# Kernel optimization log

Hardware: AMD Instinct MI355X
Metric: run time of the kernel (lower is better)

## Reference

```python
import math
import jax, jax.numpy as jnp
import numpy as np

B, S, D, H = 8, 512, 1024, 16
DH = D // H
NEG_BIG = -1.0e30  # stands in for torch's -np.inf (exp underflows to 0 identically)


def setup_inputs() -> dict:
    key0 = jax.random.key(0)
    ks = jax.random.split(key0, 20)
    n = lambda k, shp, s=1.0: jax.random.normal(k, shp, dtype=jnp.float32) * s
    inp = {}
    inp["query"] = n(ks[0], (B, S, D))
    inp["key"] = n(ks[1], (B, S, D))
    inp["value"] = n(ks[2], (B, S, D))
    # rel has exact zeros (they get masked to -10000 before its softmax)
    inp["rel"] = jax.random.randint(ks[3], (B, S, S), 0, 3).astype(jnp.float32)
    inp["timestamp"] = n(ks[4], (B, S, S))
    inp["l1"] = jnp.float32(0.3)
    inp["l2"] = jnp.float32(0.3)
    # causal mask: True = masked (future positions)
    inp["mask"] = jnp.broadcast_to(jnp.triu(jnp.ones((S, S), dtype=bool), k=1), (B, S, S))
    inp["encode_pos"] = 0
    # three qkv projection linears (total_size -> total_size)
    w = 1.0 / math.sqrt(D)
    inp["Wq"], inp["bq"] = n(ks[5], (D, D), w), jnp.zeros((D,), jnp.float32)
    inp["Wk"], inp["bk"] = n(ks[6], (D, D), w), jnp.zeros((D,), jnp.float32)
    inp["Wv"], inp["bv"] = n(ks[7], (D, D), w), jnp.zeros((D,), jnp.float32)
    # clip_factor / guessing_factor: Linear(head_size -> 1) applied to per-head key
    wh = 1.0 / math.sqrt(DH)
    inp["Wc"], inp["bc"] = n(ks[8], (1, DH), wh), jnp.zeros((1,), jnp.float32)
    inp["Wg"], inp["bg"] = n(ks[9], (1, DH), wh), jnp.zeros((1,), jnp.float32)
    return inp


def reference(query, key, value, rel, timestamp, l1, l2, mask, encode_pos,
              Wq, bq, Wk, bk, Wv, bv, Wc, bc, Wg, bg):
    b, s, d = query.shape
    dh = Wc.shape[1]
    h = d // dh

    def proj(x, W, bias):  # [b,s,d] -> [b,h,s,dh]
        return (x @ W.T + bias).reshape(b, s, h, dh).transpose(0, 2, 1, 3)

    q = proj(query, Wq, bq)
    k = proj(key, Wk, bk)
    v = proj(value, Wv, bv)

    m4 = mask[:, None]          # [b,1,s,s] broadcast over heads
    rel4 = rel[:, None]         # [b,1,s,s]
    ts4 = timestamp[:, None]    # [b,1,s,s]

    # relative softmax: zeros masked to -10000
    rel_attn = jax.nn.softmax(jnp.where(rel4 == 0, -10000.0, rel4), axis=-1)

    # scaled dot-product scores
    scores = jnp.einsum('bhqd,bhkd->bhqk', q, k) / math.sqrt(dh)
    scores = jnp.where(m4, -1.0e9, scores)

    # clip / guessing factors from per-head key -> [b,h,s,1]
    cf = k @ Wc.T + bc
    gf = k @ Wg.T + bg
    R1 = jax.nn.sigmoid(gf - cf) + gf

    # time-decay softmax
    time_stamp = jnp.where(m4, NEG_BIG, jnp.exp(-jnp.abs(ts4)))
    Rs = time_stamp + R1  # [b,h,s,s] (R1 broadcasts over last axis, as in torch)

    prob_attn = jax.nn.softmax(scores, axis=-1)
    time_attn = jax.nn.softmax(Rs, axis=-1)
    prob_attn = (1.0 - l2) * prob_attn + l2 * time_attn
    prob_attn = (1.0 - l1) * prob_attn + l1 * rel_attn

    out = jnp.einsum('bhqk,bhkd->bhqd', prob_attn, v)
    out = out.transpose(0, 2, 1, 3).reshape(b, s, d)
    return out, prob_attn
```

## Files before the change

kernel.cpp:

```cpp
#include <hip/hip_runtime.h>
#include <math.h>

typedef __attribute__((ext_vector_type(8))) short short8;
typedef __attribute__((ext_vector_type(4))) float f32x4;

#define B_  8
#define S_  512
#define D_  1024
#define H_  16
#define DH_ 64

__device__ __forceinline__ unsigned short f2bf(float f) {
    unsigned int u = __float_as_uint(f);
    u += 0x7FFFu + ((u >> 16) & 1u);
    return (unsigned short)(u >> 16);
}
__device__ __forceinline__ float bf2f(unsigned short u) {
    return __uint_as_float(((unsigned int)u) << 16);
}
__device__ __forceinline__ void gload_lds16(const void* g, void* l) {
    __builtin_amdgcn_global_load_lds(
        (const __attribute__((address_space(1))) unsigned int*)g,
        (__attribute__((address_space(3))) unsigned int*)l, 16, 0, 0);
}

__global__ __launch_bounds__(256) void conv_bf16(
    const float* __restrict__ q, const float* __restrict__ k, const float* __restrict__ v,
    const float* __restrict__ wq, const float* __restrict__ wk, const float* __restrict__ wv,
    unsigned short* __restrict__ Abf, unsigned short* __restrict__ Wbf)
{
    const size_t NA = 1048576;
    const size_t NW = 262144;
    const size_t total = 3*NA + 3*NW;
    for (size_t i4 = (size_t)blockIdx.x*blockDim.x + threadIdx.x; i4 < total;
         i4 += (size_t)gridDim.x*blockDim.x) {
        const float* s; unsigned short* d; size_t off;
        if (i4 < 3*NA) {
            const int z = (int)(i4 / NA);
            s = (z == 0) ? q : (z == 1) ? k : v;
            off = i4 - (size_t)z*NA;
            d = Abf + (size_t)z*NA*4;
        } else {
            const size_t j = i4 - 3*NA;
            const int z = (int)(j / NW);
            s = (z == 0) ? wq : (z == 1) ? wk : wv;
            off = j - (size_t)z*NW;
            d = Wbf + (size_t)z*NW*4;
        }
        const float4 f = ((const float4*)s)[off];
        ushort4 u; u.x = f2bf(f.x); u.y = f2bf(f.y); u.z = f2bf(f.z); u.w = f2bf(f.w);
        ((ushort4*)d)[off] = u;
    }
}

__global__ __launch_bounds__(256) void qkv_gemm(
    const unsigned short* __restrict__ Abf, const unsigned short* __restrict__ Wbf,
    const float* __restrict__ bq, const float* __restrict__ bk, const float* __restrict__ bv,
    unsigned short* __restrict__ qw, unsigned short* __restrict__ kw,
    unsigned short* __restrict__ vtw)
{
    __shared__ unsigned short As[128][64];
    __shared__ unsigned short Bs[128][64];

    const int bid = blockIdx.x;
    const int wid = (bid & 7) * 96 + (bid >> 3);
    const int z   = wid >> 8;
    const int rem = wid & 255;
    const int bm  = (rem >> 3) * 128;
    const int bn  = (rem & 7) * 128;

    const unsigned short* A = Abf + (size_t)z * 4194304;
    const unsigned short* W = Wbf + (size_t)z * 1048576;
    const float* bias = (z == 0) ? bq : (z == 1) ? bk : bv;
    const float scale = (z == 0) ? 0.125f : 1.0f;

    const int t = threadIdx.x, w = t >> 6, l = t & 63, lr = l & 15, lg = l >> 4;
    const int wr = (w >> 1) * 64, wc = (w & 1) * 64;

    const int srow = t >> 3;
    const int scol = 8 * ((t & 7) ^ (srow & 7));
    const unsigned short* Ast = A + (size_t)(bm + srow) * 1024 + scol;
    const unsigned short* Wst = W + (size_t)(bn + srow) * 1024 + scol;
    char* AsB = (char*)As; char* BsB = (char*)Bs;

    f32x4 acc[4][4] = {};
    for (int k0 = 0; k0 < 1024; k0 += 64) {
        __syncthreads();
        #pragma unroll
        for (int j = 0; j < 4; j++) {
            gload_lds16(Ast + (size_t)(32*j)*1024 + k0, AsB + 4096*j + t*16);
            gload_lds16(Wst + (size_t)(32*j)*1024 + k0, BsB + 4096*j + t*16);
        }
        __syncthreads();
        #pragma unroll
        for (int s = 0; s < 2; s++) {
            short8 af[4], bf4[4];
            #pragma unroll
            for (int i = 0; i < 4; i++) {
                const int row = wr + 16*i + lr;
                af[i] = *(const short8*)(AsB + row*128 + (((4*s + lg) ^ (row & 7)) << 4));
            }
            #pragma unroll
            for (int j = 0; j < 4; j++) {
                const int row = wc + 16*j + lr;
                bf4[j] = *(const short8*)(BsB + row*128 + (((4*s + lg) ^ (row & 7)) << 4));
            }
            #pragma unroll
            for (int i = 0; i < 4; i++)
                #pragma unroll
                for (int j = 0; j < 4; j++)
                    acc[i][j] = __builtin_amdgcn_mfma_f32_16x16x32_bf16(af[i], bf4[j], acc[i][j], 0, 0, 0);
        }
    }

    if (z < 2) {
        unsigned short* outp = (z == 0) ? qw : kw;
        #pragma unroll
        for (int j = 0; j < 4; j++) {
            const int n = bn + wc + 16*j + lr;
            const float bvx = bias[n];
            const int h = n >> 6, dh = n & 63;
            #pragma unroll
            for (int i = 0; i < 4; i++)
                #pragma unroll
                for (int r = 0; r < 4; r++) {
                    const int m = bm + wr + 16*i + 4*lg + r;
                    const int bb = m >> 9, s = m & 511;
                    outp[(((size_t)(bb*H_ + h))*S_ + s)*DH_ + dh] = f2bf((acc[i][j][r] + bvx) * scale);
                }
        }
    } else {
        #pragma unroll
        for (int j = 0; j < 4; j++) {
            const int n = bn + wc + 16*j + lr;
            const float bvx = bias[n];
            const int h = n >> 6, dh = n & 63;
            #pragma unroll
            for (int i = 0; i < 4; i++) {
                const int m0 = bm + wr + 16*i + 4*lg;
                const int bb = m0 >> 9, s0 = m0 & 511;
                ushort4 u;
                u.x = f2bf(acc[i][j][0] + bvx); u.y = f2bf(acc[i][j][1] + bvx);
                u.z = f2bf(acc[i][j][2] + bvx); u.w = f2bf(acc[i][j][3] + bvx);
                *(ushort4*)&vtw[(((size_t)(bb*H_ + h))*DH_ + dh)*S_ + s0] = u;
            }
        }
    }
}

__global__ __launch_bounds__(256) void e_kernel(
    const float* __restrict__ rel, const float* __restrict__ tsp,
    const float* __restrict__ pl1, const float* __restrict__ pl2,
    unsigned short* __restrict__ E)
{
    const int t = threadIdx.x, w = t >> 6, l = t & 63;
    const int ridx = blockIdx.x * 4 + w;
    const int q = ridx & (S_ - 1);
    const float l1 = *pl1, l2 = *pl2;
    const float c_t = (1.f - l1) * l2, c_r = l1;
    const float* tr = tsp + (size_t)ridx * S_;
    const float* rr = rel + (size_t)ridx * S_;

    float tv[8], rv[8]; float st = 0.f, sr = 0.f;
    #pragma unroll
    for (int j = 0; j < 8; j++) {
        const int k = l + 64*j;
        const float rvv = rr[k];
        rv[j] = (rvv != 0.f) ? __expf(rvv) : 0.f;
        sr += rv[j];
        float tvv = 0.f;
        if (k <= q) tvv = __expf(__expf(-fabsf(tr[k])));
        tv[j] = tvv; st += tvv;
    }
    #pragma unroll
    for (int m = 32; m; m >>= 1) { st += __shfl_xor(st, m); sr += __shfl_xor(sr, m); }
    const float ti   = c_t / st;
    const float riv  = (sr > 0.f) ? c_r / sr : 0.f;
    const float runi = (sr > 0.f) ? 0.f : c_r / (float)S_;

    unsigned short* Er = E + (size_t)ridx * S_;
    #pragma unroll
    for (int j = 0; j < 8; j++) {
        const int k = l + 64*j;
        Er[k] = f2bf(tv[j]*ti + rv[j]*riv + runi);
    }
}

__global__ __launch_bounds__(256) void attn_mfma(
    const unsigned short* __restrict__ qw, const unsigned short* __restrict__ kw,
    const unsigned short* __restrict__ vtw, const unsigned short* __restrict__ E,
    const float* __restrict__ pl1, const float* __restrict__ pl2,
    float* __restrict__ out, float* __restrict__ prob)
{
    __shared__ unsigned short Ps[2][64][72];

    const int t = threadIdx.x, w = t >> 6, l = t & 63, lr = l & 15, lg = l >> 4;
    const int bid = blockIdx.x;
    const int j   = bid >> 3;
    const int bh  = (bid & 7) * 16 + (j & 15);
    const int b   = bh >> 4, h = bh & 15;
    const int q0  = (j >> 4) * 64;
    const float l1 = *pl1, l2 = *pl2;
    const float c_p = (1.f - l1) * (1.f - l2);
    const unsigned short* qp = qw + (size_t)bh * (S_ * DH_);
    const unsigned short* kp = kw + (size_t)bh * (S_ * DH_);
    const unsigned short* vt = vtw + (size_t)bh * (DH_ * S_);

    short8 qa[2];
    #pragma unroll
    for (int s = 0; s < 2; s++)
        qa[s] = *(const short8*)&qp[(size_t)(q0 + 16*w + lr)*DH_ + 32*s + 8*lg];

    const int qrb = q0 + 16*w + 4*lg;

    unsigned int scp[8][4][2];
    #pragma unroll
    for (int ch = 0; ch < 8; ch++) {
        f32x4 a4[4] = {};
        #pragma unroll
        for (int s = 0; s < 2; s++)
            #pragma unroll
            for (int g = 0; g < 4; g++) {
                const short8 kb = *(const short8*)&kp[(size_t)(ch*64 + 16*g + lr)*DH_ + 32*s + 8*lg];
                a4[g] = __builtin_amdgcn_mfma_f32_16x16x32_bf16(qa[s], kb, a4[g], 0, 0, 0);
            }
        #pragma unroll
        for (int g = 0; g < 4; g++) {
            const int k = 64*ch + 16*g + lr;
            const float v0 = (k <= qrb + 0) ? a4[g][0] : -1e30f;
            const float v1 = (k <= qrb + 1) ? a4[g][1] : -1e30f;
            const float v2 = (k <= qrb + 2) ? a4[g][2] : -1e30f;
            const float v3 = (k <= qrb + 3) ? a4[g][3] : -1e30f;
            scp[ch][g][0] = ((unsigned)f2bf(v1) << 16) | f2bf(v0);
            scp[ch][g][1] = ((unsigned)f2bf(v3) << 16) | f2bf(v2);
        }
    }

    float mx[4] = {-1e30f, -1e30f, -1e30f, -1e30f};
    #pragma unroll
    for (int ch = 0; ch < 8; ch++)
        #pragma unroll
        for (int g = 0; g < 4; g++) {
            const unsigned u0 = scp[ch][g][0], u1 = scp[ch][g][1];
            mx[0] = fmaxf(mx[0], __uint_as_float(u0 << 16));
            mx[1] = fmaxf(mx[1], __uint_as_float(u0 & 0xffff0000u));
            mx[2] = fmaxf(mx[2], __uint_as_float(u1 << 16));
            mx[3] = fmaxf(mx[3], __uint_as_float(u1 & 0xffff0000u));
        }
    #pragma unroll
    for (int i = 0; i < 4; i++)
        #pragma unroll
        for (int m = 8; m; m >>= 1) mx[i] = fmaxf(mx[i], __shfl_xor(mx[i], m));

    float sm[4] = {0.f, 0.f, 0.f, 0.f};
    #pragma unroll
    for (int ch = 0; ch < 8; ch++)
        #pragma unroll
        for (int g = 0; g < 4; g++) {
            const unsigned u0 = scp[ch][g][0], u1 = scp[ch][g][1];
            const float e0 = __expf(__uint_as_float(u0 << 16)          - mx[0]);
            const float e1 = __expf(__uint_as_float(u0 & 0xffff0000u) - mx[1]);
            const float e2 = __expf(__uint_as_float(u1 << 16)          - mx[2]);
            const float e3 = __expf(__uint_as_float(u1 & 0xffff0000u) - mx[3]);
            sm[0] += e0; sm[1] += e1; sm[2] += e2; sm[3] += e3;
            scp[ch][g][0] = ((unsigned)f2bf(e1) << 16) | f2bf(e0);
            scp[ch][g][1] = ((unsigned)f2bf(e3) << 16) | f2bf(e2);
        }
    #pragma unroll
    for (int i = 0; i < 4; i++)
        #pragma unroll
        for (int m = 8; m; m >>= 1) sm[i] += __shfl_xor(sm[i], m);
    float pinv[4];
    #pragma unroll
    for (int i = 0; i < 4; i++) pinv[i] = c_p / sm[i];

    f32x4 pv[4] = {};
    const unsigned short* Eb = E + ((size_t)b * S_ + qrb) * S_;
    float* pr = prob + ((size_t)bh * S_ + qrb) * S_;
    const int prow = 16*w + 4*lg;

    #pragma unroll
    for (int ch = 0; ch < 8; ch++) {
        const int p = ch & 1;
        #pragma unroll
        for (int g = 0; g < 4; g++) {
            const int kc = 16*g + lr;
            const unsigned u0 = scp[ch][g][0], u1 = scp[ch][g][1];
            const size_t eb = (size_t)(64*ch + kc);
            const float f0 = __uint_as_float(u0 << 16)          * pinv[0] + bf2f(Eb[eb]);
            const float f1 = __uint_as_float(u0 & 0xffff0000u) * pinv[1] + bf2f(Eb[eb + 512]);
            const float f2 = __uint_as_float(u1 << 16)          * pinv[2] + bf2f(Eb[eb + 1024]);
            const float f3 = __uint_as_float(u1 & 0xffff0000u) * pinv[3] + bf2f(Eb[eb + 1536]);
            Ps[p][prow + 0][kc] = f2bf(f0);
            Ps[p][prow + 1][kc] = f2bf(f1);
            Ps[p][prow + 2][kc] = f2bf(f2);
            Ps[p][prow + 3][kc] = f2bf(f3);
            __builtin_nontemporal_store(f0, &pr[eb]);
            __builtin_nontemporal_store(f1, &pr[eb + 512]);
            __builtin_nontemporal_store(f2, &pr[eb + 1024]);
            __builtin_nontemporal_store(f3, &pr[eb + 1536]);
        }
        __syncthreads();
        #pragma unroll
        for (int s = 0; s < 2; s++) {
            const short8 pa = *(const short8*)&Ps[p][16*w + lr][32*s + 8*lg];
            #pragma unroll
            for (int g = 0; g < 4; g++) {
                const short8 vb = *(const short8*)&vt[(size_t)(16*g + lr)*S_ + 64*ch + 32*s + 8*lg];
                pv[g] = __builtin_amdgcn_mfma_f32_16x16x32_bf16(pa, vb, pv[g], 0, 0, 0);
            }
        }
    }

    #pragma unroll
    for (int g = 0; g < 4; g++)
        #pragma unroll
        for (int i = 0; i < 4; i++)
            __builtin_nontemporal_store(pv[g][i],
                &out[((size_t)(b*S_ + qrb + i))*D_ + h*DH_ + 16*g + lr]);
}

extern "C" void kernel_launch(void* const* d_in, const int* in_sizes, int n_in,
                              void* d_out, int out_size, void* d_ws, size_t ws_size,
                              hipStream_t stream)
{
    const float* query = (const float*)d_in[0];
    const float* key   = (const float*)d_in[1];
    const float* value = (const float*)d_in[2];
    const float* rel   = (const float*)d_in[3];
    const float* tsp   = (const float*)d_in[4];
    const float* l1    = (const float*)d_in[5];
    const float* l2    = (const float*)d_in[6];
    const float* Wq = (const float*)d_in[9];
    const float* bq = (const float*)d_in[10];
    const float* Wk = (const float*)d_in[11];
    const float* bk = (const float*)d_in[12];
    const float* Wv = (const float*)d_in[13];
    const float* bv = (const float*)d_in[14];

    float* out  = (float*)d_out;
    float* prob = (float*)d_out + (size_t)B_ * S_ * D_;

    unsigned short* Abf = (unsigned short*)prob;

    const size_t headN = (size_t)B_ * H_ * S_ * DH_;
    unsigned short* Wbf = (unsigned short*)d_ws;
    unsigned short* qw  = Wbf + 3*1048576;
    unsigned short* kw  = qw + headN;
    unsigned short* vtw = kw + headN;
    unsigned short* Ew  = vtw + headN;

    conv_bf16<<<2048, 256, 0, stream>>>(query, key, value, Wq, Wk, Wv, Abf, Wbf);

    qkv_gemm<<<768, 256, 0, stream>>>(Abf, Wbf, bq, bk, bv, qw, kw, vtw);

    e_kernel<<<(B_ * S_) / 4, 256, 0, stream>>>(rel, tsp, l1, l2, Ew);

    attn_mfma<<<1024, 256, 0, stream>>>(qw, kw, vtw, Ew, l1, l2, out, prob);
}
```

Before: 135.0 us.

## Fuse fp32 activation conversion into QKV GEMM and coalesce prob stores

```diff
diff --git a/kernel.cpp b/kernel.cpp
--- a/kernel.cpp
+++ b/kernel.cpp
@@ -18,48 +18,41 @@
 __device__ __forceinline__ float bf2f(unsigned short u) {
     return __uint_as_float(((unsigned int)u) << 16);
 }
+__device__ __forceinline__ unsigned cvtpk(float lo, float hi) {
+    unsigned r;
+    asm("v_cvt_pk_bf16_f32 %0, %1, %2" : "=v"(r) : "v"(lo), "v"(hi));
+    return r;
+}
 __device__ __forceinline__ void gload_lds16(const void* g, void* l) {
     __builtin_amdgcn_global_load_lds(
         (const __attribute__((address_space(1))) unsigned int*)g,
         (__attribute__((address_space(3))) unsigned int*)l, 16, 0, 0);
 }
 
-__global__ __launch_bounds__(256) void conv_bf16(
-    const float* __restrict__ q, const float* __restrict__ k, const float* __restrict__ v,
+__global__ __launch_bounds__(256) void conv_w(
     const float* __restrict__ wq, const float* __restrict__ wk, const float* __restrict__ wv,
-    unsigned short* __restrict__ Abf, unsigned short* __restrict__ Wbf)
-{
-    const size_t NA = 1048576;
+    unsigned short* __restrict__ Wbf)
+{
     const size_t NW = 262144;
-    const size_t total = 3*NA + 3*NW;
-    for (size_t i4 = (size_t)blockIdx.x*blockDim.x + threadIdx.x; i4 < total;
+    for (size_t i4 = (size_t)blockIdx.x*blockDim.x + threadIdx.x; i4 < 3*NW;
          i4 += (size_t)gridDim.x*blockDim.x) {
-        const float* s; unsigned short* d; size_t off;
-        if (i4 < 3*NA) {
-            const int z = (int)(i4 / NA);
-            s = (z == 0) ? q : (z == 1) ? k : v;
-            off = i4 - (size_t)z*NA;
-            d = Abf + (size_t)z*NA*4;
-        } else {
-            const size_t j = i4 - 3*NA;
-            const int z = (int)(j / NW);
-            s = (z == 0) ? wq : (z == 1) ? wk : wv;
-            off = j - (size_t)z*NW;
-            d = Wbf + (size_t)z*NW*4;
-        }
+        const int z = (int)(i4 / NW);
+        const float* s = (z == 0) ? wq : (z == 1) ? wk : wv;
+        const size_t off = i4 - (size_t)z*NW;
         const float4 f = ((const float4*)s)[off];
         ushort4 u; u.x = f2bf(f.x); u.y = f2bf(f.y); u.z = f2bf(f.z); u.w = f2bf(f.w);
-        ((ushort4*)d)[off] = u;
+        ((ushort4*)(Wbf + (size_t)z*NW*4))[off] = u;
     }
 }
 
 __global__ __launch_bounds__(256) void qkv_gemm(
-    const unsigned short* __restrict__ Abf, const unsigned short* __restrict__ Wbf,
+    const float* __restrict__ Aq, const float* __restrict__ Ak, const float* __restrict__ Av,
+    const unsigned short* __restrict__ Wbf,
     const float* __restrict__ bq, const float* __restrict__ bk, const float* __restrict__ bv,
     unsigned short* __restrict__ qw, unsigned short* __restrict__ kw,
     unsigned short* __restrict__ vtw)
 {
-    __shared__ unsigned short As[128][64];
+    __shared__ float As[128][64];
     __shared__ unsigned short Bs[128][64];
 
     const int bid = blockIdx.x;
@@ -69,7 +62,7 @@
     const int bm  = (rem >> 3) * 128;
     const int bn  = (rem & 7) * 128;
 
-    const unsigned short* A = Abf + (size_t)z * 4194304;
+    const float* A = (z == 0) ? Aq : (z == 1) ? Ak : Av;
     const unsigned short* W = Wbf + (size_t)z * 1048576;
     const float* bias = (z == 0) ? bq : (z == 1) ? bk : bv;
     const float scale = (z == 0) ? 0.125f : 1.0f;
@@ -77,20 +70,23 @@
     const int t = threadIdx.x, w = t >> 6, l = t & 63, lr = l & 15, lg = l >> 4;
     const int wr = (w >> 1) * 64, wc = (w & 1) * 64;
 
-    const int srow = t >> 3;
-    const int scol = 8 * ((t & 7) ^ (srow & 7));
-    const unsigned short* Ast = A + (size_t)(bm + srow) * 1024 + scol;
-    const unsigned short* Wst = W + (size_t)(bn + srow) * 1024 + scol;
+    const int srowA = t >> 4, sblkA = t & 15;
+    const float* AstA = A + (size_t)(bm + srowA) * 1024 + 4 * (sblkA ^ (srowA & 7));
+    const int srowW = t >> 3;
+    const int scolW = 8 * ((t & 7) ^ (srowW & 7));
+    const unsigned short* Wst = W + (size_t)(bn + srowW) * 1024 + scolW;
     char* AsB = (char*)As; char* BsB = (char*)Bs;
+    const float4* Af = (const float4*)As;
 
     f32x4 acc[4][4] = {};
     for (int k0 = 0; k0 < 1024; k0 += 64) {
         __syncthreads();
         #pragma unroll
-        for (int j = 0; j < 4; j++) {
-            gload_lds16(Ast + (size_t)(32*j)*1024 + k0, AsB + 4096*j + t*16);
+        for (int j = 0; j < 8; j++)
+            gload_lds16(AstA + (size_t)(16*j)*1024 + k0, AsB + 4096*j + t*16);
+        #pragma unroll
+        for (int j = 0; j < 4; j++)
             gload_lds16(Wst + (size_t)(32*j)*1024 + k0, BsB + 4096*j + t*16);
-        }
         __syncthreads();
         #pragma unroll
         for (int s = 0; s < 2; s++) {
@@ -98,7 +94,13 @@
             #pragma unroll
             for (int i = 0; i < 4; i++) {
                 const int row = wr + 16*i + lr;
-                af[i] = *(const short8*)(AsB + row*128 + (((4*s + lg) ^ (row & 7)) << 4));
+                const int b0 = 8*s + 2*lg;
+                const float4 lo = Af[row*16 + (b0      ^ (row & 7))];
+                const float4 hi = Af[row*16 + ((b0+1)  ^ (row & 7))];
+                union { uint4 u; short8 s8; } cv;
+                cv.u.x = cvtpk(lo.x, lo.y); cv.u.y = cvtpk(lo.z, lo.w);
+                cv.u.z = cvtpk(hi.x, hi.y); cv.u.w = cvtpk(hi.z, hi.w);
+                af[i] = cv.s8;
             }
             #pragma unroll
             for (int j = 0; j < 4; j++) {
@@ -276,8 +278,8 @@
 
     f32x4 pv[4] = {};
     const unsigned short* Eb = E + ((size_t)b * S_ + qrb) * S_;
-    float* pr = prob + ((size_t)bh * S_ + qrb) * S_;
     const int prow = 16*w + 4*lg;
+    const int rr = t >> 2, cg = (t & 3) << 4;
 
     #pragma unroll
     for (int ch = 0; ch < 8; ch++) {
@@ -287,18 +289,10 @@
             const int kc = 16*g + lr;
             const unsigned u0 = scp[ch][g][0], u1 = scp[ch][g][1];
             const size_t eb = (size_t)(64*ch + kc);
-            const float f0 = __uint_as_float(u0 << 16)          * pinv[0] + bf2f(Eb[eb]);
-            const float f1 = __uint_as_float(u0 & 0xffff0000u) * pinv[1] + bf2f(Eb[eb + 512]);
-            const float f2 = __uint_as_float(u1 << 16)          * pinv[2] + bf2f(Eb[eb + 1024]);
-            const float f3 = __uint_as_float(u1 & 0xffff0000u) * pinv[3] + bf2f(Eb[eb + 1536]);
-            Ps[p][prow + 0][kc] = f2bf(f0);
-            Ps[p][prow + 1][kc] = f2bf(f1);
-            Ps[p][prow + 2][kc] = f2bf(f2);
-            Ps[p][prow + 3][kc] = f2bf(f3);
-            __builtin_nontemporal_store(f0, &pr[eb]);
-            __builtin_nontemporal_store(f1, &pr[eb + 512]);
-            __builtin_nontemporal_store(f2, &pr[eb + 1024]);
-            __builtin_nontemporal_store(f3, &pr[eb + 1536]);
+            Ps[p][prow + 0][kc] = f2bf(__uint_as_float(u0 << 16)          * pinv[0] + bf2f(Eb[eb]));
+            Ps[p][prow + 1][kc] = f2bf(__uint_as_float(u0 & 0xffff0000u) * pinv[1] + bf2f(Eb[eb + 512]));
+            Ps[p][prow + 2][kc] = f2bf(__uint_as_float(u1 << 16)          * pinv[2] + bf2f(Eb[eb + 1024]));
+            Ps[p][prow + 3][kc] = f2bf(__uint_as_float(u1 & 0xffff0000u) * pinv[3] + bf2f(Eb[eb + 1536]));
         }
         __syncthreads();
         #pragma unroll
@@ -308,6 +302,17 @@
             for (int g = 0; g < 4; g++) {
                 const short8 vb = *(const short8*)&vt[(size_t)(16*g + lr)*S_ + 64*ch + 32*s + 8*lg];
                 pv[g] = __builtin_amdgcn_mfma_f32_16x16x32_bf16(pa, vb, pv[g], 0, 0, 0);
+            }
+        }
+        {
+            const unsigned short* psr = &Ps[p][rr][cg];
+            float* prp = prob + ((size_t)bh * S_ + q0 + rr) * S_ + 64*ch + cg;
+            #pragma unroll
+            for (int jj = 0; jj < 4; jj++) {
+                f32x4 f;
+                f.x = bf2f(psr[4*jj + 0]); f.y = bf2f(psr[4*jj + 1]);
+                f.z = bf2f(psr[4*jj + 2]); f.w = bf2f(psr[4*jj + 3]);
+                __builtin_nontemporal_store(f, (f32x4*)&prp[4*jj]);
             }
         }
     }
@@ -341,8 +346,6 @@
     float* out  = (float*)d_out;
     float* prob = (float*)d_out + (size_t)B_ * S_ * D_;
 
-    unsigned short* Abf = (unsigned short*)prob;
-
     const size_t headN = (size_t)B_ * H_ * S_ * DH_;
     unsigned short* Wbf = (unsigned short*)d_ws;
     unsigned short* qw  = Wbf + 3*1048576;
@@ -350,9 +353,10 @@
     unsigned short* vtw = kw + headN;
     unsigned short* Ew  = vtw + headN;
 
-    conv_bf16<<<2048, 256, 0, stream>>>(query, key, value, Wq, Wk, Wv, Abf, Wbf);
-
-    qkv_gemm<<<768, 256, 0, stream>>>(Abf, Wbf, bq, bk, bv, qw, kw, vtw);
+    conv_w<<<512, 256, 0, stream>>>(Wq, Wk, Wv, Wbf);
+
+    qkv_gemm<<<768, 256, 0, stream>>>(query, key, value, Wbf,
+                                      bq, bk, bv, qw, kw, vtw);
 
     e_kernel<<<(B_ * S_) / 4, 256, 0, stream>>>(rel, tsp, l1, l2, Ew);
 
```

New measurement: 294.8 us. +118.3%, slower.
